# Performance work log

Hardware: AMD Instinct MI355X
Metric: run time of the kernel (lower is better)

Reference implementation:

```python
import jax, jax.numpy as jnp
import numpy as np

N = 100_000      # total nodes (1000 graphs x 100 nodes)
E = 1_600_000    # total edges (avg degree 16)
B = 1_000        # ego nodes == batch size
IN_G, HID, H1, HFC, HMLP = 16, 64, 3, 128, 128
D_SENS, D_TGT, D_AREA = 64, 32, 32
OUT_S, OUT_C = 6, 8


def _seg_softmax(e, dst, n):
    # softmax over incoming edges of each destination node; e: [E,H,1]
    m = jax.ops.segment_max(e, dst, num_segments=n)
    ex = jnp.exp(e - m[dst])
    s = jax.ops.segment_sum(ex, dst, num_segments=n)
    return ex / s[dst]


def _egat(feat, efeat, src, dst, Wni, Wnj, Wfij, Wnode, attn, bias, H, d_node, d_edge):
    # DGL EGATConv: f_out = leaky_relu(f_ni[src] + f_nj[dst] + f_fij + bias)
    n = feat.shape[0]
    f_ni = feat @ Wni.T                      # [N, H*d_edge]
    f_nj = feat @ Wnj.T                      # [N, H*d_edge]
    f_e = efeat @ Wfij.T                     # [E, H*d_edge]
    f_out = f_ni[src] + f_nj[dst] + f_e + bias
    f_out = jax.nn.leaky_relu(f_out, 0.01).reshape(-1, H, d_edge)
    e = (f_out * attn).sum(-1, keepdims=True)   # [E,H,1]
    a = _seg_softmax(e, dst, n)                  # edge softmax by dst
    ft = (feat @ Wnode.T).reshape(n, H, d_node)
    h = jax.ops.segment_sum(ft[src] * a, dst, num_segments=n)  # [N,H,d_node]
    return h, f_out


def _ln(x, gamma, beta, eps=1e-5):
    mu = x.mean(-1, keepdims=True)
    v = ((x - mu) ** 2).mean(-1, keepdims=True)
    return (x - mu) * jax.lax.rsqrt(v + eps) * gamma + beta


def setup_inputs() -> dict:
    key = jax.random.key(0)
    ks = jax.random.split(key, 30)
    ego_idx = jnp.arange(0, N, N // B, dtype=jnp.int32)   # one ego node per graph
    feat = jax.random.normal(ks[0], (N, IN_G), jnp.float32)
    feat = feat.at[:, 5].set(0.0).at[ego_idx, 5].set(1.0)  # ego flag column
    enorm = jax.random.uniform(ks[1], (E, 1), dtype=jnp.float32)
    src = jax.random.randint(ks[2], (E,), 0, N, jnp.int32)
    dst = jax.random.randint(ks[3], (E,), 0, N, jnp.int32)
    sensor = jax.random.normal(ks[4], (B, D_SENS), jnp.float32)
    target = jax.random.normal(ks[5], (B, 1, D_TGT), jnp.float32)
    area = jax.random.normal(ks[6], (B, 1, D_AREA), jnp.float32)

    def w(k, o, i):
        return jax.random.normal(k, (o, i), jnp.float32) / np.sqrt(i).astype(np.float32)

    p = {
        'Wni1': w(ks[7], H1, IN_G), 'Wnj1': w(ks[8], H1, IN_G),
        'Wfij1': w(ks[9], H1, 1), 'Wnode1': w(ks[10], H1 * HID, IN_G),
        'attn1': jax.random.normal(ks[11], (1, H1, 1), jnp.float32),
        'bias1': jnp.zeros((H1,), jnp.float32),
        'Wni3': w(ks[12], 1, H1 * HID), 'Wnj3': w(ks[13], 1, H1 * HID),
        'Wfij3': w(ks[14], 1, H1), 'Wnode3': w(ks[15], HFC, H1 * HID),
        'attn3': jax.random.normal(ks[16], (1, 1, 1), jnp.float32),
        'bias3': jnp.zeros((1,), jnp.float32),
        'Ws1': w(ks[17], HMLP, D_SENS), 'bs1': jnp.zeros((HMLP,), jnp.float32),
        'Ws3': w(ks[18], HFC, HMLP), 'bs3': jnp.zeros((HFC,), jnp.float32),
        'Wt1': w(ks[19], HMLP, D_TGT + D_AREA), 'bt1': jnp.zeros((HMLP,), jnp.float32),
        'Wt2': w(ks[20], HFC, HMLP), 'bt2': jnp.zeros((HFC,), jnp.float32),
        'gM': jnp.ones((HMLP,), jnp.float32), 'bM': jnp.zeros((HMLP,), jnp.float32),
        'gF': jnp.ones((HFC,), jnp.float32), 'bF': jnp.zeros((HFC,), jnp.float32),
        'Wfc': w(ks[21], HFC, 3 * HFC), 'bfc': jnp.zeros((HFC,), jnp.float32),
        'Wst': w(ks[22], OUT_S, HFC), 'bst': jnp.zeros((OUT_S,), jnp.float32),
        'Wca': w(ks[23], OUT_C, HFC), 'bca': jnp.zeros((OUT_C,), jnp.float32),
    }
    return {'feat': feat, 'enorm': enorm, 'sensor': sensor, 'target': target,
            'area': area, 'src': src, 'dst': dst, 'ego_idx': ego_idx, **p}


def reference(feat, enorm, sensor, target, area, src, dst, ego_idx,
              Wni1, Wnj1, Wfij1, Wnode1, attn1, bias1,
              Wni3, Wnj3, Wfij3, Wnode3, attn3, bias3,
              Ws1, bs1, Ws3, bs3, Wt1, bt1, Wt2, bt2,
              gM, bM, gF, bF, Wfc, bfc, Wst, bst, Wca, bca):
    relu = jax.nn.relu
    # --- EGAT stack (dropout p=0 -> identity) ---
    hG, hE = _egat(feat, enorm, src, dst, Wni1, Wnj1, Wfij1, Wnode1, attn1, bias1,
                   H1, HID, 1)
    hG = relu(hG.reshape(-1, H1 * HID))          # [N, 192]
    hE = hE.reshape(-1, H1 * 1)                   # [E, 3]
    hG, hE = _egat(hG, hE, src, dst, Wni3, Wnj3, Wfij3, Wnode3, attn3, bias3,
                   1, HFC, 1)
    hG = relu(hG.reshape(-1, HFC))                # [N, 128]
    hGraph = hG[ego_idx]                          # [B, 128] (feat[:,5]==1 nodes)
    # --- sensor MLP ---
    hS = relu(_ln(sensor @ Ws1.T + bs1, gM, bM))
    hS = relu(_ln(hS @ Ws3.T + bs3, gM, bM))
    # --- target MLP ---
    hTA = jnp.concatenate([target[:, 0, :], area[:, 0, :]], axis=1)  # [B, 64]
    hT = relu(_ln(hTA @ Wt1.T + bt1, gM, bM))
    hT = relu(_ln(hT @ Wt2.T + bt2, gM, bM))
    # --- fusion + heads ---
    h = jnp.concatenate([hGraph, hS, hT], axis=1)  # [B, 384]
    h = relu(_ln(h @ Wfc.T + bfc, gF, bF))
    return (h @ Wst.T + bst, h @ Wca.T + bca)
```

## Files before the change

kernel.cpp:

```cpp
#include <hip/hip_runtime.h>
#include <cstdint>

#define N_NODES 100000
#define N_EDGES 1600000
#define N_BATCH 1000
#define LEAK 0.01f
#define RSTRIDE 64
#define PREB 391
#define TWB 480
#define EGO_STRIDE 100

#define OFF_S1 0
#define OFF_S3 8192
#define OFF_T1 24576
#define OFF_T2 32768
#define OFF_N3 49152
#define OFF_FC 73728
#define WT_TOTAL 122880

__device__ __forceinline__ float lrelu(float x){ return x > 0.f ? x : LEAK * x; }
__device__ __forceinline__ float expw(float x){ return __expf(fminf(x, 80.f)); }
__device__ __forceinline__ int is_ego(int n){ return (n % EGO_STRIDE) == 0; }


__global__ void k_mark_pre(const int* __restrict__ src, const int* __restrict__ dst,
                           int* __restrict__ Sflag,
                           const float* __restrict__ feat,
                           const float* __restrict__ Wni1, const float* __restrict__ Wnj1,
                           float4* __restrict__ fni1p, float4* __restrict__ fnj1p,
                           const float* __restrict__ Ws1, const float* __restrict__ Ws3,
                           const float* __restrict__ Wt1, const float* __restrict__ Wt2,
                           const float* __restrict__ Wnode3, const float* __restrict__ Wfc,
                           float* __restrict__ wsWT){
  if (blockIdx.x < PREB){
    int n = blockIdx.x * 256 + threadIdx.x;
    if (n >= N_NODES) return;
    const float4* f4 = (const float4*)(feat + (size_t)n * 16);
    float4 a = f4[0], b = f4[1], c = f4[2], d = f4[3];
    float f[16] = {a.x,a.y,a.z,a.w, b.x,b.y,b.z,b.w, c.x,c.y,c.z,c.w, d.x,d.y,d.z,d.w};
    float ni[3], nj[3];
    #pragma unroll
    for (int h = 0; h < 3; h++){
      float s0 = 0.f, s1 = 0.f;
      #pragma unroll
      for (int k = 0; k < 16; k++){ s0 += f[k] * Wni1[h * 16 + k]; s1 += f[k] * Wnj1[h * 16 + k]; }
      ni[h] = s0; nj[h] = s1;
    }
    fni1p[n] = make_float4(ni[0], ni[1], ni[2], 0.f);
    fnj1p[n] = make_float4(nj[0], nj[1], nj[2], 0.f);
    return;
  }
  if (blockIdx.x < PREB + TWB){
    int gi = (blockIdx.x - PREB) * 256 + threadIdx.x;
    if (gi < 8192){            int i = gi;          int o = i >> 6,  c = i & 63;       wsWT[OFF_S1 + c * 128 + o] = Ws1[i]; }
    else if (gi < 24576){      int i = gi - 8192;   int o = i >> 7,  c = i & 127;      wsWT[OFF_S3 + c * 128 + o] = Ws3[i]; }
    else if (gi < 32768){      int i = gi - 24576;  int o = i >> 6,  c = i & 63;       wsWT[OFF_T1 + c * 128 + o] = Wt1[i]; }
    else if (gi < 49152){      int i = gi - 32768;  int o = i >> 7,  c = i & 127;      wsWT[OFF_T2 + c * 128 + o] = Wt2[i]; }
    else if (gi < 73728){      int i = gi - 49152;  int o = i / 192, c = i - o * 192;  wsWT[OFF_N3 + c * 128 + o] = Wnode3[i]; }
    else {                     int i = gi - 73728;  int o = i / 384, c = i - o * 384;  wsWT[OFF_FC + c * 128 + o] = Wfc[i]; }
    return;
  }
  int e4 = (blockIdx.x - PREB - TWB) * 256 + threadIdx.x;
  if (e4 >= N_EDGES / 4) return;
  int4 d = ((const int4*)dst)[e4];
  int f0 = is_ego(d.x), f1 = is_ego(d.y), f2 = is_ego(d.z), f3 = is_ego(d.w);
  if (f0 | f1 | f2 | f3){
    int4 s = ((const int4*)src)[e4];
    if (f0) Sflag[s.x] = 1;
    if (f1) Sflag[s.y] = 1;
    if (f2) Sflag[s.z] = 1;
    if (f3) Sflag[s.w] = 1;
  }
}

__global__ void k_compact(const int* __restrict__ Sflag, int* __restrict__ nodeslot,
                          int* __restrict__ S_ids, int* __restrict__ meta){
  int n = blockIdx.x * blockDim.x + threadIdx.x;
  if (n < N_NODES && (Sflag[n] | is_ego(n))){
    int s = atomicAdd(&meta[0], 1);
    S_ids[s] = n; nodeslot[n] = s + 1;
  }
}

__global__ void k_fill(const int* __restrict__ src, const int* __restrict__ dst,
                       const float* __restrict__ enorm,
                       const int* __restrict__ nodeslot, int* __restrict__ cursor,
                       int2* __restrict__ edata){
  int e4 = blockIdx.x * blockDim.x + threadIdx.x;
  if (e4 >= N_EDGES / 4) return;
  int4 d = ((const int4*)dst)[e4];
  int4 s = ((const int4*)src)[e4];
  float4 en = ((const float4*)enorm)[e4];
  int dd[4] = {d.x, d.y, d.z, d.w};
  int ss[4] = {s.x, s.y, s.z, s.w};
  float ee[4] = {en.x, en.y, en.z, en.w};
  #pragma unroll
  for (int u = 0; u < 4; u++){
    int ns = nodeslot[dd[u]];
    if (ns > 0){
      int sl = ns - 1;
      int p = atomicAdd(&cursor[sl], 1);
      if (p < RSTRIDE) edata[sl * RSTRIDE + p] = make_int2(ss[u], __float_as_int(ee[u]));
    }
  }
}


__global__ __launch_bounds__(256) void k6f(
    const float* __restrict__ feat, const float4* __restrict__ fni1p, const float4* __restrict__ fnj1p,
    const int* __restrict__ S_ids, const int* __restrict__ cursor,
    const int2* __restrict__ edata,
    const float* __restrict__ Wnode1, const float* __restrict__ Wfij1,
    const float* __restrict__ attn1, const float* __restrict__ bias1,
    const float* __restrict__ Wni3, const float* __restrict__ Wnj3,
    const int* __restrict__ meta, float* __restrict__ hG_S,
    float* __restrict__ fni3_S, float* __restrict__ fnj3_S)
{
  __shared__ float Wn1[192 * 17];
  const int t = threadIdx.x;
  for (int i = t; i < 3072; i += 256) Wn1[(i >> 4) * 17 + (i & 15)] = Wnode1[i];
  __syncthreads();
  const int S = meta[0];
  int lane = t & 63;
  int wid = blockIdx.x * 4 + (t >> 6);
  int nw = gridDim.x * 4;
  float wf0 = Wfij1[0], wf1 = Wfij1[1], wf2 = Wfij1[2];
  float at0 = attn1[0], at1 = attn1[1], at2 = attn1[2];
  float b0 = bias1[0], b1 = bias1[1], b2 = bias1[2];
  float wi3a = Wni3[lane], wi3b = Wni3[64 + lane], wi3c = Wni3[128 + lane];
  float wj3a = Wnj3[lane], wj3b = Wnj3[64 + lane], wj3c = Wnj3[128 + lane];
  const int e = lane & 15, cg = lane >> 4;

  for (int s = wid; s < S; s += nw){
    int n = S_ids[s];
    int len = min(cursor[s], RSTRIDE);
    long long j0 = (long long)s * RSTRIDE;
    float4 fj = fnj1p[n];
    float ls0 = 0.f, ls1 = 0.f, ls2 = 0.f;
    float ws[3][4];
    #pragma unroll
    for (int h = 0; h < 3; h++)
      #pragma unroll
      for (int k = 0; k < 4; k++) ws[h][k] = 0.f;

    for (int base = 0; base < len; base += 16){
      int idx = base + e;
      if (idx < len){
        int2 ed = edata[j0 + idx];
        int sn = ed.x; float en = __int_as_float(ed.y);
        float4 fi = fni1p[sn];
        float l0 = lrelu(fi.x + fj.x + en * wf0 + b0);
        float l1 = lrelu(fi.y + fj.y + en * wf1 + b1);
        float l2 = lrelu(fi.z + fj.z + en * wf2 + b2);
        float w0 = expw(l0 * at0), w1 = expw(l1 * at1), w2 = expw(l2 * at2);
        ls0 += w0; ls1 += w1; ls2 += w2;
        const float4 f4 = *(const float4*)(feat + (size_t)sn * 16 + cg * 4);
        float fv[4] = {f4.x, f4.y, f4.z, f4.w};
        #pragma unroll
        for (int k = 0; k < 4; k++){
          ws[0][k] += w0 * fv[k];
          ws[1][k] += w1 * fv[k];
          ws[2][k] += w2 * fv[k];
        }
      }
    }
    #pragma unroll
    for (int off = 1; off < 16; off <<= 1){
      ls0 += __shfl_xor(ls0, off);
      ls1 += __shfl_xor(ls1, off);
      ls2 += __shfl_xor(ls2, off);
      #pragma unroll
      for (int h = 0; h < 3; h++)
        #pragma unroll
        for (int k = 0; k < 4; k++) ws[h][k] += __shfl_xor(ws[h][k], off);
    }
    float inv0 = (len > 0) ? 1.f / ls0 : 0.f;
    float inv1 = (len > 0) ? 1.f / ls1 : 0.f;
    float inv2 = (len > 0) ? 1.f / ls2 : 0.f;
    float aval[3][4];
    #pragma unroll
    for (int k = 0; k < 4; k++){
      aval[0][k] = ws[0][k] * inv0;
      aval[1][k] = ws[1][k] * inv1;
      aval[2][k] = ws[2][k] * inv2;
    }
    float hv[3];
    #pragma unroll
    for (int h = 0; h < 3; h++){
      float acc = 0.f;
      #pragma unroll
      for (int q = 0; q < 4; q++)
        #pragma unroll
        for (int k = 0; k < 4; k++)
          acc += __shfl(aval[h][k], q * 16) * Wn1[(h * 64 + lane) * 17 + q * 4 + k];
      hv[h] = fmaxf(acc, 0.f);
      hG_S[(long long)s * 192 + h * 64 + lane] = hv[h];
    }
    float ni = hv[0] * wi3a + hv[1] * wi3b + hv[2] * wi3c;
    float nj = hv[0] * wj3a + hv[1] * wj3b + hv[2] * wj3c;
    #pragma unroll
    for (int off = 32; off > 0; off >>= 1){
      ni += __shfl_xor(ni, off);
      nj += __shfl_xor(nj, off);
    }
    if (lane == 0){ fni3_S[s] = ni; fnj3_S[s] = nj; }
  }
}


__device__ __forceinline__ void ln1(float& f0, float gv, float bv, float* red, int lane, int wv, int p){
  float a0 = f0;
  #pragma unroll
  for (int off = 32; off > 0; off >>= 1) a0 += __shfl_xor(a0, off);
  if (lane == 0) red[wv] = a0;
  __syncthreads();
  float s0 = red[2 * p] + red[2 * p + 1];
  __syncthreads();
  float d0 = f0 - s0 * (1.f / 128.f);
  a0 = d0 * d0;
  #pragma unroll
  for (int off = 32; off > 0; off >>= 1) a0 += __shfl_xor(a0, off);
  if (lane == 0) red[wv] = a0;
  __syncthreads();
  float q0 = red[2 * p] + red[2 * p + 1];
  __syncthreads();
  f0 = fmaxf(0.f, d0 * rsqrtf(q0 * (1.f / 128.f) + 1e-5f) * gv + bv);
}

template<int K>
__device__ __forceinline__ float dotg(const float* __restrict__ WT, const float* __restrict__ x, int o){
  float z0 = 0.f, z1 = 0.f, z2 = 0.f, z3 = 0.f;
  #pragma unroll 4
  for (int c = 0; c < K; c += 4){
    z0 += WT[(c + 0) * 128 + o] * x[c + 0];
    z1 += WT[(c + 1) * 128 + o] * x[c + 1];
    z2 += WT[(c + 2) * 128 + o] * x[c + 2];
    z3 += WT[(c + 3) * 128 + o] * x[c + 3];
  }
  return (z0 + z1) + (z2 + z3);
}

__global__ __launch_bounds__(256) void k8f(
    const int* __restrict__ ego, const int* __restrict__ nodeslot, const int* __restrict__ cursor,
    const int2* __restrict__ edata,
    const float4* __restrict__ fni1p, const float4* __restrict__ fnj1p,
    const float* __restrict__ fni3_S, const float* __restrict__ fnj3_S,
    const float* __restrict__ hG_S, const float* __restrict__ wsWT,
    const float* __restrict__ Wfij1, const float* __restrict__ attn1, const float* __restrict__ bias1,
    const float* __restrict__ Wfij3, const float* __restrict__ attn3, const float* __restrict__ bias3,
    const float* __restrict__ sensor, const float* __restrict__ target, const float* __restrict__ area,
    const float* __restrict__ bs1, const float* __restrict__ bs3,
    const float* __restrict__ bt1, const float* __restrict__ bt2,
    const float* __restrict__ gM, const float* __restrict__ bM,
    const float* __restrict__ gF, const float* __restrict__ bF,
    const float* __restrict__ bfc,
    const float* __restrict__ Wst, const float* __restrict__ bst,
    const float* __restrict__ Wca, const float* __restrict__ bca,
    float* __restrict__ out)
{
  __shared__ float agg[2 * 192];
  __shared__ float xc2[2 * 384];
  __shared__ float act[2 * 64];
  __shared__ float hbuf[2 * 128];
  __shared__ float Wlf[128 * 15];
  __shared__ float red[8];
  const int t = threadIdx.x;
  const int lane = t & 63, wv = t >> 6;
  const int o = t & 127, p = t >> 7;
  const int b0 = blockIdx.x * 2;
  const float g_m = gM[o], b_m = bM[o];

  if (wv < 2){
    int b = b0 + wv;
    int n = ego[b];
    int slot = nodeslot[n] - 1;
    int len = min(cursor[slot], RSTRIDE);
    long long j0 = (long long)slot * RSTRIDE;
    float wf0 = Wfij1[0], wf1 = Wfij1[1], wf2 = Wfij1[2];
    float bb0 = bias1[0], bb1 = bias1[1], bb2 = bias1[2];
    float g0 = Wfij3[0], g1 = Wfij3[1], g2 = Wfij3[2];
    float at3 = attn3[0], bb3 = bias3[0];
    float4 fj = fnj1p[n];
    float fnj3v = fnj3_S[slot];

    float lsum = 0.f;
    float acc[3] = {0.f, 0.f, 0.f};
    for (int base = 0; base < len; base += 64){
      int j = base + lane;
      float w = 0.f; int ss = 0;
      if (j < len){
        int2 ed = edata[j0 + j];
        int sn = ed.x; float en = __int_as_float(ed.y);
        float4 fi = fni1p[sn];
        float l0 = lrelu(fi.x + fj.x + en * wf0 + bb0);
        float l1 = lrelu(fi.y + fj.y + en * wf1 + bb1);
        float l2 = lrelu(fi.z + fj.z + en * wf2 + bb2);
        float fe3 = l0 * g0 + l1 * g1 + l2 * g2;
        ss = nodeslot[sn] - 1;
        float l3 = lrelu(fni3_S[ss] + fnj3v + fe3 + bb3);
        w = expw(l3 * at3);
        lsum += w;
      }
      int c2 = min(64, len - base);
      for (int i0 = 0; i0 < c2; i0 += 4){
        float wvv[4], fr[4][3];
        #pragma unroll
        for (int u = 0; u < 4; u++){
          int idx = i0 + u;
          int s2 = __shfl(ss, idx);
          wvv[u] = __shfl(w, idx);
          bool ok = idx < c2;
          #pragma unroll
          for (int r = 0; r < 3; r++)
            fr[u][r] = ok ? hG_S[(long long)s2 * 192 + r * 64 + lane] : 0.f;
          if (!ok) wvv[u] = 0.f;
        }
        #pragma unroll
        for (int u = 0; u < 4; u++)
          #pragma unroll
          for (int r = 0; r < 3; r++) acc[r] += wvv[u] * fr[u][r];
      }
    }
    #pragma unroll
    for (int off = 32; off > 0; off >>= 1) lsum += __shfl_xor(lsum, off);
    float inv = (len > 0) ? 1.f / lsum : 0.f;
    #pragma unroll
    for (int r = 0; r < 3; r++) agg[wv * 192 + r * 64 + lane] = acc[r] * inv;
  } else {
    int i0 = t - 128;
    {
      int r = i0 >> 6, c = i0 & 63;
      act[i0] = sensor[(b0 + r) * 64 + c];
    }
    for (int i = i0; i < 14 * 128; i += 128){
      int oo = i >> 7, cc = i & 127;
      Wlf[cc * 15 + oo] = (oo < 6) ? Wst[oo * 128 + cc] : Wca[(oo - 6) * 128 + cc];
    }
  }
  __syncthreads();

  float z = bs1[o] + dotg<64>(wsWT + OFF_S1, act + p * 64, o);
  ln1(z, g_m, b_m, red, lane, wv, p);
  hbuf[p * 128 + o] = z;
  __syncthreads();

  z = bs3[o] + dotg<128>(wsWT + OFF_S3, hbuf + p * 128, o);
  ln1(z, g_m, b_m, red, lane, wv, p);
  xc2[p * 384 + 128 + o] = z;

  for (int i = t; i < 128; i += 256){
    int r = i >> 6, c = i & 63;
    act[i] = (c < 32) ? target[(b0 + r) * 32 + c] : area[(b0 + r) * 32 + c - 32];
  }
  __syncthreads();

  z = bt1[o] + dotg<64>(wsWT + OFF_T1, act + p * 64, o);
  ln1(z, g_m, b_m, red, lane, wv, p);
  hbuf[p * 128 + o] = z;
  __syncthreads();

  z = bt2[o] + dotg<128>(wsWT + OFF_T2, hbuf + p * 128, o);
  ln1(z, g_m, b_m, red, lane, wv, p);
  xc2[p * 384 + 256 + o] = z;
  __syncthreads();

  z = dotg<192>(wsWT + OFF_N3, agg + p * 192, o);
  xc2[p * 384 + o] = fmaxf(0.f, z);
  __syncthreads();

  float fz = bfc[o] + dotg<384>(wsWT + OFF_FC, xc2 + p * 384, o);
  ln1(fz, gF[o], bF[o], red, lane, wv, p);

  float* v1 = agg;
  v1[p * 128 + o] = fz;
  __syncthreads();
  if (o < 14){
    float a0 = (o < 6) ? bst[o] : bca[o - 6];
    #pragma unroll 8
    for (int c = 0; c < 128; c++) a0 += Wlf[c * 15 + o] * v1[p * 128 + c];
    int e0 = b0 + p;
    if (o < 6) out[e0 * 6 + o] = a0;
    else       out[N_BATCH * 6 + e0 * 8 + o - 6] = a0;
  }
}


extern "C" void kernel_launch(void* const* d_in, const int* in_sizes, int n_in,
                              void* d_out, int out_size, void* d_ws, size_t ws_size,
                              hipStream_t stream)
{
  const float* feat   = (const float*)d_in[0];
  const float* enorm  = (const float*)d_in[1];
  const float* sensor = (const float*)d_in[2];
  const float* target = (const float*)d_in[3];
  const float* area   = (const float*)d_in[4];
  const int*   src    = (const int*)d_in[5];
  const int*   dst    = (const int*)d_in[6];
  const int*   ego    = (const int*)d_in[7];
  const float* Wni1   = (const float*)d_in[8];
  const float* Wnj1   = (const float*)d_in[9];
  const float* Wfij1  = (const float*)d_in[10];
  const float* Wnode1 = (const float*)d_in[11];
  const float* attn1  = (const float*)d_in[12];
  const float* bias1  = (const float*)d_in[13];
  const float* Wni3   = (const float*)d_in[14];
  const float* Wnj3   = (const float*)d_in[15];
  const float* Wfij3  = (const float*)d_in[16];
  const float* Wnode3 = (const float*)d_in[17];
  const float* attn3  = (const float*)d_in[18];
  const float* bias3  = (const float*)d_in[19];
  const float* Ws1    = (const float*)d_in[20];
  const float* bs1    = (const float*)d_in[21];
  const float* Ws3    = (const float*)d_in[22];
  const float* bs3    = (const float*)d_in[23];
  const float* Wt1    = (const float*)d_in[24];
  const float* bt1    = (const float*)d_in[25];
  const float* Wt2    = (const float*)d_in[26];
  const float* bt2    = (const float*)d_in[27];
  const float* gM     = (const float*)d_in[28];
  const float* bM     = (const float*)d_in[29];
  const float* gF     = (const float*)d_in[30];
  const float* bF     = (const float*)d_in[31];
  const float* Wfc    = (const float*)d_in[32];
  const float* bfc    = (const float*)d_in[33];
  const float* Wst    = (const float*)d_in[34];
  const float* bst    = (const float*)d_in[35];
  const float* Wca    = (const float*)d_in[36];
  const float* bca    = (const float*)d_in[37];
  float* out = (float*)d_out;

  char* ws = (char*)d_ws;
  size_t off = 0;
  auto alloc = [&](size_t bytes) -> size_t {
    size_t o = off;
    off = (off + bytes + 255) & ~(size_t)255;
    return o;
  };

  size_t o_meta    = alloc(256);
  size_t o_Sflag   = alloc((size_t)N_NODES * 4);
  size_t o_nodeslot= alloc((size_t)N_NODES * 4);
  size_t o_cursor  = alloc((size_t)N_NODES * 4);
  size_t zero_bytes = off;
  size_t o_fni1p   = alloc((size_t)N_NODES * 16);
  size_t o_fnj1p   = alloc((size_t)N_NODES * 16);
  size_t o_S_ids   = alloc((size_t)N_NODES * 4);
  size_t o_fni3    = alloc((size_t)N_NODES * 4);
  size_t o_fnj3    = alloc((size_t)N_NODES * 4);
  size_t o_wsWT    = alloc((size_t)WT_TOTAL * 4);
  size_t rem = (ws_size > off) ? ws_size - off : 0;
  size_t scap = rem / (RSTRIDE * 8 + 768);
  if (scap > (size_t)N_NODES) scap = N_NODES;
  if (scap < 1) scap = 1;
  size_t o_edata = alloc(scap * RSTRIDE * 8);
  size_t o_hG_S  = alloc(scap * 768);

  int*    meta      = (int*)(ws + o_meta);
  int*    Sflag     = (int*)(ws + o_Sflag);
  int*    nodeslot  = (int*)(ws + o_nodeslot);
  int*    cursor    = (int*)(ws + o_cursor);
  float4* fni1p     = (float4*)(ws + o_fni1p);
  float4* fnj1p     = (float4*)(ws + o_fnj1p);
  int*    S_ids     = (int*)(ws + o_S_ids);
  float*  fni3_S    = (float*)(ws + o_fni3);
  float*  fnj3_S    = (float*)(ws + o_fnj3);
  float*  wsWT      = (float*)(ws + o_wsWT);
  int2*   edata     = (int2*)(ws + o_edata);
  float*  hG_S      = (float*)(ws + o_hG_S);

  hipMemsetAsync(ws, 0, zero_bytes, stream);

  k_mark_pre<<<PREB + TWB + (N_EDGES / 4 + 255) / 256, 256, 0, stream>>>(
      src, dst, Sflag, feat, Wni1, Wnj1, fni1p, fnj1p,
      Ws1, Ws3, Wt1, Wt2, Wnode3, Wfc, wsWT);
  k_compact<<<(N_NODES + 255) / 256, 256, 0, stream>>>(Sflag, nodeslot, S_ids, meta);
  k_fill<<<(N_EDGES / 4 + 255) / 256, 256, 0, stream>>>(src, dst, enorm, nodeslot, cursor, edata);
  k6f<<<2048, 256, 0, stream>>>(feat, fni1p, fnj1p, S_ids, cursor, edata,
                                Wnode1, Wfij1, attn1, bias1, Wni3, Wnj3, meta,
                                hG_S, fni3_S, fnj3_S);
  k8f<<<N_BATCH / 2, 256, 0, stream>>>(ego, nodeslot, cursor, edata, fni1p, fnj1p,
                                       fni3_S, fnj3_S, hG_S, wsWT,
                                       Wfij1, attn1, bias1, Wfij3, attn3, bias3,
                                       sensor, target, area, bs1, bs3, bt1, bt2,
                                       gM, bM, gF, bF, bfc, Wst, bst, Wca, bca, out);
  (void)in_sizes; (void)n_in; (void)out_size;
}
```

Measured before the change: 249.2 us.

## Drop node compaction; index edge buckets and hidden states directly by node id

Removes the k_compact kernel and the nodeslot/S_ids indirection, so edge buckets, hG_S and the layer-3 projections are addressed by global node id, with the Sflag/ego test done inline. This cuts one kernel launch and an atomic-counter compaction pass, plus a dependent gather in k_fill and k8f. In exchange, k6f now scans all 100k nodes and skips unflagged ones, and the workspace grows to full-size edata (N*64*8 bytes) and hG_S (N*768 bytes) with no capacity check. That could exceed the workspace, and the sparse layout costs some locality.

New measurement: 243.3 us. 1.02x faster.

```diff
diff --git a/kernel.cpp b/kernel.cpp
--- a/kernel.cpp
+++ b/kernel.cpp
@@ -73,34 +73,31 @@
   }
 }
 
-__global__ void k_compact(const int* __restrict__ Sflag, int* __restrict__ nodeslot,
-                          int* __restrict__ S_ids, int* __restrict__ meta){
-  int n = blockIdx.x * blockDim.x + threadIdx.x;
-  if (n < N_NODES && (Sflag[n] | is_ego(n))){
-    int s = atomicAdd(&meta[0], 1);
-    S_ids[s] = n; nodeslot[n] = s + 1;
-  }
-}
-
 __global__ void k_fill(const int* __restrict__ src, const int* __restrict__ dst,
                        const float* __restrict__ enorm,
-                       const int* __restrict__ nodeslot, int* __restrict__ cursor,
+                       const int* __restrict__ Sflag, int* __restrict__ cursor,
                        int2* __restrict__ edata){
   int e4 = blockIdx.x * blockDim.x + threadIdx.x;
   if (e4 >= N_EDGES / 4) return;
   int4 d = ((const int4*)dst)[e4];
+  int dd[4] = {d.x, d.y, d.z, d.w};
+  int cand[4];
+  int any = 0;
+  #pragma unroll
+  for (int u = 0; u < 4; u++){
+    cand[u] = Sflag[dd[u]] | is_ego(dd[u]);
+    any |= cand[u];
+  }
+  if (!any) return;
   int4 s = ((const int4*)src)[e4];
   float4 en = ((const float4*)enorm)[e4];
-  int dd[4] = {d.x, d.y, d.z, d.w};
   int ss[4] = {s.x, s.y, s.z, s.w};
   float ee[4] = {en.x, en.y, en.z, en.w};
   #pragma unroll
   for (int u = 0; u < 4; u++){
-    int ns = nodeslot[dd[u]];
-    if (ns > 0){
-      int sl = ns - 1;
-      int p = atomicAdd(&cursor[sl], 1);
-      if (p < RSTRIDE) edata[sl * RSTRIDE + p] = make_int2(ss[u], __float_as_int(ee[u]));
+    if (cand[u]){
+      int p = atomicAdd(&cursor[dd[u]], 1);
+      if (p < RSTRIDE) edata[(long long)dd[u] * RSTRIDE + p] = make_int2(ss[u], __float_as_int(ee[u]));
     }
   }
 }
@@ -108,19 +105,17 @@
 
 __global__ __launch_bounds__(256) void k6f(
     const float* __restrict__ feat, const float4* __restrict__ fni1p, const float4* __restrict__ fnj1p,
-    const int* __restrict__ S_ids, const int* __restrict__ cursor,
+    const int* __restrict__ Sflag, const int* __restrict__ cursor,
     const int2* __restrict__ edata,
     const float* __restrict__ Wnode1, const float* __restrict__ Wfij1,
     const float* __restrict__ attn1, const float* __restrict__ bias1,
     const float* __restrict__ Wni3, const float* __restrict__ Wnj3,
-    const int* __restrict__ meta, float* __restrict__ hG_S,
-    float* __restrict__ fni3_S, float* __restrict__ fnj3_S)
+    float* __restrict__ hG_S, float* __restrict__ fni3_S, float* __restrict__ fnj3_S)
 {
   __shared__ float Wn1[192 * 17];
   const int t = threadIdx.x;
   for (int i = t; i < 3072; i += 256) Wn1[(i >> 4) * 17 + (i & 15)] = Wnode1[i];
   __syncthreads();
-  const int S = meta[0];
   int lane = t & 63;
   int wid = blockIdx.x * 4 + (t >> 6);
   int nw = gridDim.x * 4;
@@ -131,10 +126,10 @@
   float wj3a = Wnj3[lane], wj3b = Wnj3[64 + lane], wj3c = Wnj3[128 + lane];
   const int e = lane & 15, cg = lane >> 4;
 
-  for (int s = wid; s < S; s += nw){
-    int n = S_ids[s];
-    int len = min(cursor[s], RSTRIDE);
-    long long j0 = (long long)s * RSTRIDE;
+  for (int n = wid; n < N_NODES; n += nw){
+    if (!(Sflag[n] | is_ego(n))) continue;
+    int len = min(cursor[n], RSTRIDE);
+    long long j0 = (long long)n * RSTRIDE;
     float4 fj = fnj1p[n];
     float ls0 = 0.f, ls1 = 0.f, ls2 = 0.f;
     float ws[3][4];
@@ -194,7 +189,7 @@
         for (int k = 0; k < 4; k++)
           acc += __shfl(aval[h][k], q * 16) * Wn1[(h * 64 + lane) * 17 + q * 4 + k];
       hv[h] = fmaxf(acc, 0.f);
-      hG_S[(long long)s * 192 + h * 64 + lane] = hv[h];
+      hG_S[(long long)n * 192 + h * 64 + lane] = hv[h];
     }
     float ni = hv[0] * wi3a + hv[1] * wi3b + hv[2] * wi3c;
     float nj = hv[0] * wj3a + hv[1] * wj3b + hv[2] * wj3c;
@@ -203,7 +198,7 @@
       ni += __shfl_xor(ni, off);
       nj += __shfl_xor(nj, off);
     }
-    if (lane == 0){ fni3_S[s] = ni; fnj3_S[s] = nj; }
+    if (lane == 0){ fni3_S[n] = ni; fnj3_S[n] = nj; }
   }
 }
 
@@ -241,7 +236,7 @@
 }
 
 __global__ __launch_bounds__(256) void k8f(
-    const int* __restrict__ ego, const int* __restrict__ nodeslot, const int* __restrict__ cursor,
+    const int* __restrict__ ego, const int* __restrict__ cursor,
     const int2* __restrict__ edata,
     const float4* __restrict__ fni1p, const float4* __restrict__ fnj1p,
     const float* __restrict__ fni3_S, const float* __restrict__ fnj3_S,
@@ -273,15 +268,14 @@
   if (wv < 2){
     int b = b0 + wv;
     int n = ego[b];
-    int slot = nodeslot[n] - 1;
-    int len = min(cursor[slot], RSTRIDE);
-    long long j0 = (long long)slot * RSTRIDE;
+    int len = min(cursor[n], RSTRIDE);
+    long long j0 = (long long)n * RSTRIDE;
     float wf0 = Wfij1[0], wf1 = Wfij1[1], wf2 = Wfij1[2];
     float bb0 = bias1[0], bb1 = bias1[1], bb2 = bias1[2];
     float g0 = Wfij3[0], g1 = Wfij3[1], g2 = Wfij3[2];
     float at3 = attn3[0], bb3 = bias3[0];
     float4 fj = fnj1p[n];
-    float fnj3v = fnj3_S[slot];
+    float fnj3v = fnj3_S[n];
 
     float lsum = 0.f;
     float acc[3] = {0.f, 0.f, 0.f};
@@ -296,7 +290,7 @@
         float l1 = lrelu(fi.y + fj.y + en * wf1 + bb1);
         float l2 = lrelu(fi.z + fj.z + en * wf2 + bb2);
         float fe3 = l0 * g0 + l1 * g1 + l2 * g2;
-        ss = nodeslot[sn] - 1;
+        ss = sn;
         float l3 = lrelu(fni3_S[ss] + fnj3v + fe3 + bb3);
         w = expw(l3 * at3);
         lsum += w;
@@ -437,31 +431,21 @@
     return o;
   };
 
-  size_t o_meta    = alloc(256);
   size_t o_Sflag   = alloc((size_t)N_NODES * 4);
-  size_t o_nodeslot= alloc((size_t)N_NODES * 4);
   size_t o_cursor  = alloc((size_t)N_NODES * 4);
   size_t zero_bytes = off;
   size_t o_fni1p   = alloc((size_t)N_NODES * 16);
   size_t o_fnj1p   = alloc((size_t)N_NODES * 16);
-  size_t o_S_ids   = alloc((size_t)N_NODES * 4);
   size_t o_fni3    = alloc((size_t)N_NODES * 4);
   size_t o_fnj3    = alloc((size_t)N_NODES * 4);
   size_t o_wsWT    = alloc((size_t)WT_TOTAL * 4);
-  size_t rem = (ws_size > off) ? ws_size - off : 0;
-  size_t scap = rem / (RSTRIDE * 8 + 768);
-  if (scap > (size_t)N_NODES) scap = N_NODES;
-  if (scap < 1) scap = 1;
-  size_t o_edata = alloc(scap * RSTRIDE * 8);
-  size_t o_hG_S  = alloc(scap * 768);
-
-  int*    meta      = (int*)(ws + o_meta);
+  size_t o_edata   = alloc((size_t)N_NODES * RSTRIDE * 8);
+  size_t o_hG_S    = alloc((size_t)N_NODES * 768);
+
   int*    Sflag     = (int*)(ws + o_Sflag);
-  int*    nodeslot  = (int*)(ws + o_nodeslot);
   int*    cursor    = (int*)(ws + o_cursor);
   float4* fni1p     = (float4*)(ws + o_fni1p);
   float4* fnj1p     = (float4*)(ws + o_fnj1p);
-  int*    S_ids     = (int*)(ws + o_S_ids);
   float*  fni3_S    = (float*)(ws + o_fni3);
   float*  fnj3_S    = (float*)(ws + o_fnj3);
   float*  wsWT      = (float*)(ws + o_wsWT);
@@ -473,12 +457,11 @@
   k_mark_pre<<<PREB + TWB + (N_EDGES / 4 + 255) / 256, 256, 0, stream>>>(
       src, dst, Sflag, feat, Wni1, Wnj1, fni1p, fnj1p,
       Ws1, Ws3, Wt1, Wt2, Wnode3, Wfc, wsWT);
-  k_compact<<<(N_NODES + 255) / 256, 256, 0, stream>>>(Sflag, nodeslot, S_ids, meta);
-  k_fill<<<(N_EDGES / 4 + 255) / 256, 256, 0, stream>>>(src, dst, enorm, nodeslot, cursor, edata);
-  k6f<<<2048, 256, 0, stream>>>(feat, fni1p, fnj1p, S_ids, cursor, edata,
-                                Wnode1, Wfij1, attn1, bias1, Wni3, Wnj3, meta,
+  k_fill<<<(N_EDGES / 4 + 255) / 256, 256, 0, stream>>>(src, dst, enorm, Sflag, cursor, edata);
+  k6f<<<2048, 256, 0, stream>>>(feat, fni1p, fnj1p, Sflag, cursor, edata,
+                                Wnode1, Wfij1, attn1, bias1, Wni3, Wnj3,
                                 hG_S, fni3_S, fnj3_S);
-  k8f<<<N_BATCH / 2, 256, 0, stream>>>(ego, nodeslot, cursor, edata, fni1p, fnj1p,
+  k8f<<<N_BATCH / 2, 256, 0, stream>>>(ego, cursor, edata, fni1p, fnj1p,
                                        fni3_S, fnj3_S, hG_S, wsWT,
                                        Wfij1, attn1, bias1, Wfij3, attn3, bias3,
                                        sensor, target, area, bs1, bs3, bt1, bt2,
```
